# Kernel optimization log

Hardware: AMD Instinct MI355X
Metric: run time of the kernel (lower is better)

The kernel has to match this reference:

```python
import jax, jax.numpy as jnp
import numpy as np

B, S, D = 4, 2048, 512
H = 8
HD = D // H  # 64
F = 2048
EPS = 1e-12


def _layer_norm(x, g, b):
    mu = jnp.mean(x, axis=-1, keepdims=True)
    var = jnp.mean((x - mu) ** 2, axis=-1, keepdims=True)
    return (x - mu) * jax.lax.rsqrt(var + EPS) * g + b


def setup_inputs() -> dict:
    key = jax.random.key(0)
    ks = jax.random.split(key, 16)
    sd = 0.02
    inp = {
        "x": jax.random.normal(ks[0], (B, S, D), dtype=jnp.float32),
        # per-head q/k/v projections stacked: [H, D, HD] weights, [H, HD] biases
        "Wq": jax.random.normal(ks[1], (H, D, HD), dtype=jnp.float32) * sd,
        "bq": jnp.zeros((H, HD), dtype=jnp.float32),
        "Wk": jax.random.normal(ks[2], (H, D, HD), dtype=jnp.float32) * sd,
        "bk": jnp.zeros((H, HD), dtype=jnp.float32),
        "Wv": jax.random.normal(ks[3], (H, D, HD), dtype=jnp.float32) * sd,
        "bv": jnp.zeros((H, HD), dtype=jnp.float32),
        "Wo": jax.random.normal(ks[4], (D, D), dtype=jnp.float32) * sd,
        "bo": jnp.zeros((D,), dtype=jnp.float32),
        "W1": jax.random.normal(ks[5], (D, F), dtype=jnp.float32) * sd,
        "b1": jnp.zeros((F,), dtype=jnp.float32),
        "W2": jax.random.normal(ks[6], (F, D), dtype=jnp.float32) * sd,
        "b2": jnp.zeros((D,), dtype=jnp.float32),
        "ln1_g": jnp.ones((D,), dtype=jnp.float32),
        "ln1_b": jnp.zeros((D,), dtype=jnp.float32),
        "ln2_g": jnp.ones((D,), dtype=jnp.float32),
        "ln2_b": jnp.zeros((D,), dtype=jnp.float32),
    }
    return inp


def reference(x, Wq, bq, Wk, bk, Wv, bv, Wo, bo, W1, b1, W2, b2,
              ln1_g, ln1_b, ln2_g, ln2_b):
    # Multi-head attention: per-head Linear projections, batched over heads.
    q = jnp.einsum('bsd,hde->bhse', x, Wq) + bq[None, :, None, :]
    k = jnp.einsum('bsd,hde->bhse', x, Wk) + bk[None, :, None, :]
    v = jnp.einsum('bsd,hde->bhse', x, Wv) + bv[None, :, None, :]
    scores = jnp.einsum('bhse,bhte->bhst', q, k) / jnp.sqrt(jnp.float32(HD))
    weights = jax.nn.softmax(scores, axis=-1)  # [B,H,S,S] -- dominant traffic
    attn = jnp.einsum('bhst,bhte->bhse', weights, v)
    # concat heads in order along feature dim -> [B,S,D]
    concat = jnp.transpose(attn, (0, 2, 1, 3)).reshape(B, S, D)
    attn_out = concat @ Wo + bo
    # post-LN residual 1
    x1 = _layer_norm(x + attn_out, ln1_g, ln1_b)
    # FFN (exact GELU, matching torch nn.GELU default)
    h = jax.nn.gelu(x1 @ W1 + b1, approximate=False)
    ff = h @ W2 + b2
    # post-LN residual 2
    return _layer_norm(x1 + ff, ln2_g, ln2_b)
```

## Files before the change

### kernel.cpp

```cpp
#include <hip/hip_runtime.h>
#include <math.h>

#define Bb 4
#define Ss 2048
#define Dd 512
#define Hh 8
#define HDd 64
#define Ff 2048

typedef __bf16 bf16x8 __attribute__((ext_vector_type(8)));
typedef __bf16 bf16x4 __attribute__((ext_vector_type(4)));
typedef float  f32x4  __attribute__((ext_vector_type(4)));

__device__ __forceinline__ float gelu_f(float x) {
    return 0.5f * x * (1.0f + erff(x * 0.70710678118654752440f));
}

__device__ __forceinline__ unsigned short bfbits(float f) {
    __bf16 h = (__bf16)f;
    return __builtin_bit_cast(unsigned short, h);
}

__global__ __launch_bounds__(256) void tconv_kernel(
    const float* __restrict__ in, unsigned short* __restrict__ out,
    int R, int C)
{
    __shared__ float tile[32][33];
    const size_t bo = (size_t)blockIdx.z * R * C;
    const int c0 = blockIdx.x * 32, r0 = blockIdx.y * 32;
    const int tx = threadIdx.x & 31, ty = threadIdx.x >> 5;
    #pragma unroll
    for (int rr = ty; rr < 32; rr += 8)
        tile[rr][tx] = in[bo + (size_t)(r0 + rr) * C + c0 + tx];
    __syncthreads();
    #pragma unroll
    for (int cc = ty; cc < 32; cc += 8)
        out[bo + (size_t)(c0 + cc) * R + r0 + tx] = bfbits(tile[tx][cc]);
}

__global__ __launch_bounds__(256) void f2b_kernel(
    const float* __restrict__ in, unsigned short* __restrict__ out)
{
    const size_t i = ((size_t)blockIdx.x * 256 + threadIdx.x) * 8;
    float4 a = *(const float4*)(in + i);
    float4 b = *(const float4*)(in + i + 4);
    union { unsigned short us[8]; uint4 u; } p;
    p.us[0] = bfbits(a.x); p.us[1] = bfbits(a.y);
    p.us[2] = bfbits(a.z); p.us[3] = bfbits(a.w);
    p.us[4] = bfbits(b.x); p.us[5] = bfbits(b.y);
    p.us[6] = bfbits(b.z); p.us[7] = bfbits(b.w);
    *(uint4*)(out + i) = p.u;
}

template<int ACT, int OUTBF>
__global__ __launch_bounds__(256) void gemm_mfma(
    const unsigned short* __restrict__ A, const unsigned short* __restrict__ Bt,
    const float* __restrict__ bias, void* __restrict__ C,
    int M, int N, int K)
{
    __shared__ unsigned short Asb[128][40];
    __shared__ unsigned short Bsb[128][40];
    const int t    = threadIdx.x;
    const int lane = t & 63;
    const int w    = t >> 6;
    const int ln15 = lane & 15;
    const int quad = lane >> 4;
    const int mw = (w & 1) * 64;
    const int nw = (w >> 1) * 64;
    const int m0 = blockIdx.y * 128;
    const int n0 = blockIdx.x * 128;

    f32x4 acc[4][4];
    #pragma unroll
    for (int i = 0; i < 4; i++)
        #pragma unroll
        for (int j = 0; j < 4; j++) acc[i][j] = (f32x4){0.f, 0.f, 0.f, 0.f};

    for (int k0 = 0; k0 < K; k0 += 32) {
        #pragma unroll
        for (int p = 0; p < 2; p++) {
            const int f   = t + p * 256;
            const int row = f >> 2;
            const int k8  = (f & 3) << 3;
            *(bf16x8*)&Asb[row][k8] =
                *(const bf16x8*)(A + (size_t)(m0 + row) * K + k0 + k8);
            *(bf16x8*)&Bsb[row][k8] =
                *(const bf16x8*)(Bt + (size_t)(n0 + row) * K + k0 + k8);
        }
        __syncthreads();
        bf16x8 af[4], bf[4];
        const int kcol = quad * 8;
        #pragma unroll
        for (int i = 0; i < 4; i++)
            af[i] = *(const bf16x8*)&Asb[mw + i * 16 + ln15][kcol];
        #pragma unroll
        for (int j = 0; j < 4; j++)
            bf[j] = *(const bf16x8*)&Bsb[nw + j * 16 + ln15][kcol];
        #pragma unroll
        for (int i = 0; i < 4; i++)
            #pragma unroll
            for (int j = 0; j < 4; j++)
                acc[i][j] = __builtin_amdgcn_mfma_f32_16x16x32_bf16(
                    af[i], bf[j], acc[i][j], 0, 0, 0);
        __syncthreads();
    }

    #pragma unroll
    for (int i = 0; i < 4; i++) {
        #pragma unroll
        for (int r = 0; r < 4; r++) {
            const int m = m0 + mw + i * 16 + quad * 4 + r;
            #pragma unroll
            for (int j = 0; j < 4; j++) {
                const int n = n0 + nw + j * 16 + ln15;
                float val = acc[i][j][r] + bias[n];
                if (ACT) val = gelu_f(val);
                if (OUTBF)
                    ((unsigned short*)C)[(size_t)m * N + n] = bfbits(val);
                else
                    ((float*)C)[(size_t)m * N + n] = val;
            }
        }
    }
}

__global__ __launch_bounds__(256) void qkv_mfma(
    const unsigned short* __restrict__ A,
    const unsigned short* __restrict__ WqT, const unsigned short* __restrict__ WkT,
    const unsigned short* __restrict__ WvT,
    const float* __restrict__ bq, const float* __restrict__ bk,
    const float* __restrict__ bv, unsigned short* __restrict__ qkv)
{
    const unsigned short* Bt = blockIdx.z == 0 ? WqT : (blockIdx.z == 1 ? WkT : WvT);
    const float* bias = blockIdx.z == 0 ? bq : (blockIdx.z == 1 ? bk : bv);
    unsigned short* O = qkv + (size_t)blockIdx.z * ((size_t)Bb * Hh * Ss * HDd);
    const float scl = blockIdx.z == 0 ? 0.125f : 1.0f;

    __shared__ unsigned short Asb[128][40];
    __shared__ unsigned short Bsb[128][40];
    const int t    = threadIdx.x;
    const int lane = t & 63;
    const int w    = t >> 6;
    const int ln15 = lane & 15;
    const int quad = lane >> 4;
    const int mw = (w & 1) * 64;
    const int nw = (w >> 1) * 64;
    const int m0 = blockIdx.y * 128;
    const int n0 = blockIdx.x * 128;

    f32x4 acc[4][4];
    #pragma unroll
    for (int i = 0; i < 4; i++)
        #pragma unroll
        for (int j = 0; j < 4; j++) acc[i][j] = (f32x4){0.f, 0.f, 0.f, 0.f};

    for (int k0 = 0; k0 < Dd; k0 += 32) {
        #pragma unroll
        for (int p = 0; p < 2; p++) {
            const int f   = t + p * 256;
            const int row = f >> 2;
            const int k8  = (f & 3) << 3;
            *(bf16x8*)&Asb[row][k8] =
                *(const bf16x8*)(A + (size_t)(m0 + row) * Dd + k0 + k8);
            *(bf16x8*)&Bsb[row][k8] =
                *(const bf16x8*)(Bt + (size_t)(n0 + row) * Dd + k0 + k8);
        }
        __syncthreads();
        bf16x8 af[4], bf[4];
        const int kcol = quad * 8;
        #pragma unroll
        for (int i = 0; i < 4; i++)
            af[i] = *(const bf16x8*)&Asb[mw + i * 16 + ln15][kcol];
        #pragma unroll
        for (int j = 0; j < 4; j++)
            bf[j] = *(const bf16x8*)&Bsb[nw + j * 16 + ln15][kcol];
        #pragma unroll
        for (int i = 0; i < 4; i++)
            #pragma unroll
            for (int j = 0; j < 4; j++)
                acc[i][j] = __builtin_amdgcn_mfma_f32_16x16x32_bf16(
                    af[i], bf[j], acc[i][j], 0, 0, 0);
        __syncthreads();
    }

    if (blockIdx.z == 2) {
        #pragma unroll
        for (int i = 0; i < 4; i++) {
            const int mb = m0 + mw + i * 16 + quad * 4;
            const int bI = mb >> 11;
            const int sI = mb & 2047;
            #pragma unroll
            for (int j = 0; j < 4; j++) {
                const int n = n0 + nw + j * 16 + ln15;
                union { unsigned short us[4]; uint2 u2; } pk;
                #pragma unroll
                for (int r = 0; r < 4; r++)
                    pk.us[r] = bfbits(acc[i][j][r] + bias[n]);
                *(uint2*)&O[(((size_t)bI * Hh + (n >> 6)) * HDd + (n & 63)) * Ss + sI]
                    = pk.u2;
            }
        }
    } else {
        #pragma unroll
        for (int i = 0; i < 4; i++) {
            #pragma unroll
            for (int r = 0; r < 4; r++) {
                const int m  = m0 + mw + i * 16 + quad * 4 + r;
                const int bI = m >> 11;
                const int sI = m & 2047;
                #pragma unroll
                for (int j = 0; j < 4; j++) {
                    const int n = n0 + nw + j * 16 + ln15;
                    const float val = (acc[i][j][r] + bias[n]) * scl;
                    O[(((size_t)bI * Hh + (n >> 6)) * Ss + sI) * HDd + (n & 63)] =
                        bfbits(val);
                }
            }
        }
    }
}

__global__ __launch_bounds__(256) void attn_mfma(
    const unsigned short* __restrict__ q, const unsigned short* __restrict__ k,
    const unsigned short* __restrict__ vt, unsigned short* __restrict__ out)
{
    __shared__ unsigned short Ks[64][72];
    __shared__ unsigned short VTs[64][72];
    __shared__ unsigned short Ps[64][72];
    __shared__ float alph[4][16];
    const int t    = threadIdx.x;
    const int lane = t & 63;
    const int w    = t >> 6;
    const int ln15 = lane & 15;
    const int quad = lane >> 4;
    const int qw   = w * 16;
    const int h = blockIdx.y, b = blockIdx.z;
    const int q0 = blockIdx.x * 64;
    const unsigned short* qb  = q  + (((size_t)b * Hh + h) * Ss + q0) * HDd;
    const unsigned short* kb  = k  + ((size_t)b * Hh + h) * Ss * HDd;
    const unsigned short* vtb = vt + ((size_t)b * Hh + h) * HDd * Ss;

    const bf16x8 qf0 = *(const bf16x8*)(qb + (size_t)(qw + ln15) * HDd + quad * 8);
    const bf16x8 qf1 = *(const bf16x8*)(qb + (size_t)(qw + ln15) * HDd + 32 + quad * 8);

    f32x4 o_acc[4];
    #pragma unroll
    for (int s = 0; s < 4; s++) o_acc[s] = (f32x4){0.f, 0.f, 0.f, 0.f};
    float m_run = -1e30f, l_run = 0.f;

    for (int kt = 0; kt < Ss; kt += 64) {
        __syncthreads();
        #pragma unroll
        for (int p = 0; p < 2; p++) {
            const int u = p * 256 + t;
            const int row = u >> 3, ch = u & 7;
            *(bf16x8*)&Ks[row][ch * 8] =
                *(const bf16x8*)(kb + (size_t)(kt + row) * HDd + ch * 8);
            *(bf16x8*)&VTs[row][ch * 8] =
                *(const bf16x8*)(vtb + (size_t)row * Ss + kt + ch * 8);
        }
        __syncthreads();

        f32x4 sc[4];
        #pragma unroll
        for (int s = 0; s < 4; s++) {
            const bf16x8 ka = *(const bf16x8*)&Ks[s * 16 + ln15][quad * 8];
            const bf16x8 kb2 = *(const bf16x8*)&Ks[s * 16 + ln15][32 + quad * 8];
            f32x4 z = (f32x4){0.f, 0.f, 0.f, 0.f};
            z = __builtin_amdgcn_mfma_f32_16x16x32_bf16(ka, qf0, z, 0, 0, 0);
            sc[s] = __builtin_amdgcn_mfma_f32_16x16x32_bf16(kb2, qf1, z, 0, 0, 0);
        }

        float mt = -1e30f;
        #pragma unroll
        for (int s = 0; s < 4; s++)
            #pragma unroll
            for (int r = 0; r < 4; r++) mt = fmaxf(mt, sc[s][r]);
        mt = fmaxf(mt, __shfl_xor(mt, 16));
        mt = fmaxf(mt, __shfl_xor(mt, 32));
        const float mn = fmaxf(m_run, mt);
        const float a = __expf(m_run - mn);
        float lt = 0.f;
        #pragma unroll
        for (int s = 0; s < 4; s++)
            #pragma unroll
            for (int r = 0; r < 4; r++) {
                sc[s][r] = __expf(sc[s][r] - mn);
                lt += sc[s][r];
            }
        lt += __shfl_xor(lt, 16);
        lt += __shfl_xor(lt, 32);
        l_run = l_run * a + lt;
        m_run = mn;
        if (quad == 0) alph[w][ln15] = a;

        #pragma unroll
        for (int s = 0; s < 4; s++) {
            union { unsigned short us[4]; uint2 u2; } pk;
            #pragma unroll
            for (int r = 0; r < 4; r++) pk.us[r] = bfbits(sc[s][r]);
            *(uint2*)&Ps[qw + ln15][s * 16 + quad * 4] = pk.u2;
        }

        const float4 av = *(const float4*)&alph[w][quad * 4];
        #pragma unroll
        for (int s = 0; s < 4; s++) {
            o_acc[s][0] *= av.x; o_acc[s][1] *= av.y;
            o_acc[s][2] *= av.z; o_acc[s][3] *= av.w;
        }

        const bf16x8 pf0 = *(const bf16x8*)&Ps[qw + ln15][quad * 8];
        const bf16x8 pf1 = *(const bf16x8*)&Ps[qw + ln15][32 + quad * 8];
        #pragma unroll
        for (int s = 0; s < 4; s++) {
            const bf16x8 v0 = *(const bf16x8*)&VTs[s * 16 + ln15][quad * 8];
            const bf16x8 v1 = *(const bf16x8*)&VTs[s * 16 + ln15][32 + quad * 8];
            o_acc[s] = __builtin_amdgcn_mfma_f32_16x16x32_bf16(pf0, v0, o_acc[s], 0, 0, 0);
            o_acc[s] = __builtin_amdgcn_mfma_f32_16x16x32_bf16(pf1, v1, o_acc[s], 0, 0, 0);
        }
    }

    if (quad == 0) alph[w][ln15] = l_run;
    const float4 lv = *(const float4*)&alph[w][quad * 4];
    const float inv[4] = {1.f / lv.x, 1.f / lv.y, 1.f / lv.z, 1.f / lv.w};
    #pragma unroll
    for (int r = 0; r < 4; r++) {
        const int row = q0 + qw + quad * 4 + r;
        #pragma unroll
        for (int s = 0; s < 4; s++) {
            const int dim = s * 16 + ln15;
            out[((size_t)b * Ss + row) * Dd + h * HDd + dim] =
                bfbits(o_acc[s][r] * inv[r]);
        }
    }
}

template<int WRITE_BF>
__global__ __launch_bounds__(256) void ln_kernel(
    const float* __restrict__ a, const float* __restrict__ res,
    const float* __restrict__ g, const float* __restrict__ bb,
    float* __restrict__ out, unsigned short* __restrict__ outb)
{
    const int row = blockIdx.x;
    const int t = threadIdx.x;
    const float* pa = a + (size_t)row * Dd;
    const float* pr = res + (size_t)row * Dd;
    float v0 = pa[t] + pr[t];
    float v1 = pa[t + 256] + pr[t + 256];

    float sum = v0 + v1;
    #pragma unroll
    for (int o = 32; o; o >>= 1) sum += __shfl_down(sum, o);
    __shared__ float red1[4], red2[4];
    const int wid = t >> 6, lane = t & 63;
    if (!lane) red1[wid] = sum;
    __syncthreads();
    sum = red1[0] + red1[1] + red1[2] + red1[3];
    const float mu = sum * (1.0f / Dd);

    const float d0 = v0 - mu, d1 = v1 - mu;
    float sq = d0 * d0 + d1 * d1;
    #pragma unroll
    for (int o = 32; o; o >>= 1) sq += __shfl_down(sq, o);
    if (!lane) red2[wid] = sq;
    __syncthreads();
    sq = red2[0] + red2[1] + red2[2] + red2[3];
    const float rstd = rsqrtf(sq * (1.0f / Dd) + 1e-12f);

    const float y0 = d0 * rstd * g[t] + bb[t];
    const float y1 = d1 * rstd * g[t + 256] + bb[t + 256];
    out[(size_t)row * Dd + t]       = y0;
    out[(size_t)row * Dd + t + 256] = y1;
    if (WRITE_BF) {
        outb[(size_t)row * Dd + t]       = bfbits(y0);
        outb[(size_t)row * Dd + t + 256] = bfbits(y1);
    }
}

extern "C" void kernel_launch(void* const* d_in, const int* in_sizes, int n_in,
                              void* d_out, int out_size, void* d_ws, size_t ws_size,
                              hipStream_t stream) {
    const float* x   = (const float*)d_in[0];
    const float* Wq  = (const float*)d_in[1];
    const float* bq  = (const float*)d_in[2];
    const float* Wk  = (const float*)d_in[3];
    const float* bk  = (const float*)d_in[4];
    const float* Wv  = (const float*)d_in[5];
    const float* bv  = (const float*)d_in[6];
    const float* Wo  = (const float*)d_in[7];
    const float* bo  = (const float*)d_in[8];
    const float* W1  = (const float*)d_in[9];
    const float* b1  = (const float*)d_in[10];
    const float* W2  = (const float*)d_in[11];
    const float* b2  = (const float*)d_in[12];
    const float* g1  = (const float*)d_in[13];
    const float* be1 = (const float*)d_in[14];
    const float* g2  = (const float*)d_in[15];
    const float* be2 = (const float*)d_in[16];
    float* out = (float*)d_out;

    const size_t NT = (size_t)Bb * Ss * Dd;
    unsigned short* wsu  = (unsigned short*)d_ws;
    unsigned short* qkvb = wsu;
    unsigned short* hb   = wsu + 3 * NT;
    unsigned short* actb = wsu + 7 * NT;
    unsigned short* x1b  = wsu + 8 * NT;
    float* proj = (float*)(wsu + 9 * NT);
    float* ff   = proj;
    float* x1   = proj + NT;
    unsigned short* wpool = (unsigned short*)(x1 + NT);
    unsigned short* WqT = wpool;
    unsigned short* WkT = wpool + 262144;
    unsigned short* WvT = wpool + 524288;
    unsigned short* WoT = wpool + 786432;
    unsigned short* W1T = wpool + 1048576;
    unsigned short* W2T = wpool + 2097152;
    const int M = Bb * Ss;

    tconv_kernel<<<dim3(2, 16, 8), 256, 0, stream>>>(Wq, WqT, Dd, HDd);
    tconv_kernel<<<dim3(2, 16, 8), 256, 0, stream>>>(Wk, WkT, Dd, HDd);
    tconv_kernel<<<dim3(2, 16, 8), 256, 0, stream>>>(Wv, WvT, Dd, HDd);
    tconv_kernel<<<dim3(16, 16, 1), 256, 0, stream>>>(Wo, WoT, Dd, Dd);
    tconv_kernel<<<dim3(64, 16, 1), 256, 0, stream>>>(W1, W1T, Dd, Ff);
    tconv_kernel<<<dim3(16, 64, 1), 256, 0, stream>>>(W2, W2T, Ff, Dd);

    f2b_kernel<<<2048, 256, 0, stream>>>(x, actb);
    qkv_mfma<<<dim3(Dd / 128, M / 128, 3), 256, 0, stream>>>(
        actb, WqT, WkT, WvT, bq, bk, bv, qkvb);

    attn_mfma<<<dim3(Ss / 64, Hh, Bb), 256, 0, stream>>>(
        qkvb, qkvb + NT, qkvb + 2 * NT, actb);

    gemm_mfma<0, 0><<<dim3(Dd / 128, M / 128), 256, 0, stream>>>(
        actb, WoT, bo, proj, M, Dd, Dd);

    ln_kernel<1><<<M, 256, 0, stream>>>(x, proj, g1, be1, x1, x1b);

    gemm_mfma<1, 1><<<dim3(Ff / 128, M / 128), 256, 0, stream>>>(
        x1b, W1T, b1, hb, M, Ff, Dd);
    gemm_mfma<0, 0><<<dim3(Dd / 128, M / 128), 256, 0, stream>>>(
        hb, W2T, b2, ff, M, Dd, Ff);

    ln_kernel<0><<<M, 256, 0, stream>>>(x1, ff, g2, be2, out, nullptr);
}
```

Baseline: 361.8 us.

## Merge weight-prep launches and load GEMM tiles directly into LDS

```diff
diff --git a/kernel.cpp b/kernel.cpp
--- a/kernel.cpp
+++ b/kernel.cpp
@@ -9,7 +9,6 @@
 #define Ff 2048
 
 typedef __bf16 bf16x8 __attribute__((ext_vector_type(8)));
-typedef __bf16 bf16x4 __attribute__((ext_vector_type(4)));
 typedef float  f32x4  __attribute__((ext_vector_type(4)));
 
 __device__ __forceinline__ float gelu_f(float x) {
@@ -21,35 +20,66 @@
     return __builtin_bit_cast(unsigned short, h);
 }
 
-__global__ __launch_bounds__(256) void tconv_kernel(
+__device__ __forceinline__ void gld16(const unsigned short* g, unsigned short* l) {
+    __builtin_amdgcn_global_load_lds(
+        (const __attribute__((address_space(1))) unsigned int*)g,
+        (__attribute__((address_space(3))) unsigned int*)l, 16, 0, 0);
+}
+
+__device__ __forceinline__ void tile_tconv(
     const float* __restrict__ in, unsigned short* __restrict__ out,
-    int R, int C)
+    int R, int C, int c0, int r0)
 {
     __shared__ float tile[32][33];
-    const size_t bo = (size_t)blockIdx.z * R * C;
-    const int c0 = blockIdx.x * 32, r0 = blockIdx.y * 32;
     const int tx = threadIdx.x & 31, ty = threadIdx.x >> 5;
     #pragma unroll
     for (int rr = ty; rr < 32; rr += 8)
-        tile[rr][tx] = in[bo + (size_t)(r0 + rr) * C + c0 + tx];
+        tile[rr][tx] = in[(size_t)(r0 + rr) * C + c0 + tx];
     __syncthreads();
     #pragma unroll
     for (int cc = ty; cc < 32; cc += 8)
-        out[bo + (size_t)(c0 + cc) * R + r0 + tx] = bfbits(tile[tx][cc]);
-}
-
-__global__ __launch_bounds__(256) void f2b_kernel(
-    const float* __restrict__ in, unsigned short* __restrict__ out)
-{
-    const size_t i = ((size_t)blockIdx.x * 256 + threadIdx.x) * 8;
-    float4 a = *(const float4*)(in + i);
-    float4 b = *(const float4*)(in + i + 4);
-    union { unsigned short us[8]; uint4 u; } p;
-    p.us[0] = bfbits(a.x); p.us[1] = bfbits(a.y);
-    p.us[2] = bfbits(a.z); p.us[3] = bfbits(a.w);
-    p.us[4] = bfbits(b.x); p.us[5] = bfbits(b.y);
-    p.us[6] = bfbits(b.z); p.us[7] = bfbits(b.w);
-    *(uint4*)(out + i) = p.u;
+        out[(size_t)(c0 + cc) * R + r0 + tx] = bfbits(tile[tx][cc]);
+}
+
+__global__ __launch_bounds__(256) void prep_kernel(
+    const float* __restrict__ Wq, const float* __restrict__ Wk,
+    const float* __restrict__ Wv, const float* __restrict__ Wo,
+    const float* __restrict__ W1, const float* __restrict__ W2,
+    const float* __restrict__ x,
+    unsigned short* __restrict__ WqT, unsigned short* __restrict__ WkT,
+    unsigned short* __restrict__ WvT, unsigned short* __restrict__ WoT,
+    unsigned short* __restrict__ W1T, unsigned short* __restrict__ W2T,
+    unsigned short* __restrict__ xb)
+{
+    const int bid = blockIdx.x;
+    if (bid < 768) {
+        const float* src = bid < 256 ? Wq : (bid < 512 ? Wk : Wv);
+        unsigned short* dst = bid < 256 ? WqT : (bid < 512 ? WkT : WvT);
+        const int local = bid & 255;
+        const int z = local >> 5;
+        const int rem = local & 31;
+        tile_tconv(src + (size_t)z * Dd * HDd, dst + (size_t)z * Dd * HDd,
+                   Dd, HDd, (rem & 1) * 32, (rem >> 1) * 32);
+    } else if (bid < 1024) {
+        const int local = bid - 768;
+        tile_tconv(Wo, WoT, Dd, Dd, (local & 15) * 32, (local >> 4) * 32);
+    } else if (bid < 2048) {
+        const int local = bid - 1024;
+        tile_tconv(W1, W1T, Dd, Ff, (local & 63) * 32, (local >> 6) * 32);
+    } else if (bid < 3072) {
+        const int local = bid - 2048;
+        tile_tconv(W2, W2T, Ff, Dd, (local & 15) * 32, (local >> 4) * 32);
+    } else {
+        const size_t i = ((size_t)(bid - 3072) * 256 + threadIdx.x) * 8;
+        float4 a = *(const float4*)(x + i);
+        float4 b = *(const float4*)(x + i + 4);
+        union { unsigned short us[8]; uint4 u; } p;
+        p.us[0] = bfbits(a.x); p.us[1] = bfbits(a.y);
+        p.us[2] = bfbits(a.z); p.us[3] = bfbits(a.w);
+        p.us[4] = bfbits(b.x); p.us[5] = bfbits(b.y);
+        p.us[6] = bfbits(b.z); p.us[7] = bfbits(b.w);
+        *(uint4*)(xb + i) = p.u;
+    }
 }
 
 template<int ACT, int OUTBF>
@@ -58,8 +88,8 @@
     const float* __restrict__ bias, void* __restrict__ C,
     int M, int N, int K)
 {
-    __shared__ unsigned short Asb[128][40];
-    __shared__ unsigned short Bsb[128][40];
+    __shared__ unsigned short Asb[128 * 32];
+    __shared__ unsigned short Bsb[128 * 32];
     const int t    = threadIdx.x;
     const int lane = t & 63;
     const int w    = t >> 6;
@@ -70,6 +100,9 @@
     const int m0 = blockIdx.y * 128;
     const int n0 = blockIdx.x * 128;
 
+    const int r0c = t >> 2,           ch0 = (t & 3) << 3;
+    const int r1c = (t + 256) >> 2,   ch1 = ch0;
+
     f32x4 acc[4][4];
     #pragma unroll
     for (int i = 0; i < 4; i++)
@@ -77,25 +110,19 @@
         for (int j = 0; j < 4; j++) acc[i][j] = (f32x4){0.f, 0.f, 0.f, 0.f};
 
     for (int k0 = 0; k0 < K; k0 += 32) {
-        #pragma unroll
-        for (int p = 0; p < 2; p++) {
-            const int f   = t + p * 256;
-            const int row = f >> 2;
-            const int k8  = (f & 3) << 3;
-            *(bf16x8*)&Asb[row][k8] =
-                *(const bf16x8*)(A + (size_t)(m0 + row) * K + k0 + k8);
-            *(bf16x8*)&Bsb[row][k8] =
-                *(const bf16x8*)(Bt + (size_t)(n0 + row) * K + k0 + k8);
-        }
+        gld16(A  + (size_t)(m0 + r0c) * K + k0 + ch0, &Asb[t * 8]);
+        gld16(A  + (size_t)(m0 + r1c) * K + k0 + ch1, &Asb[(t + 256) * 8]);
+        gld16(Bt + (size_t)(n0 + r0c) * K + k0 + ch0, &Bsb[t * 8]);
+        gld16(Bt + (size_t)(n0 + r1c) * K + k0 + ch1, &Bsb[(t + 256) * 8]);
         __syncthreads();
         bf16x8 af[4], bf[4];
         const int kcol = quad * 8;
         #pragma unroll
         for (int i = 0; i < 4; i++)
-            af[i] = *(const bf16x8*)&Asb[mw + i * 16 + ln15][kcol];
+            af[i] = *(const bf16x8*)&Asb[(mw + i * 16 + ln15) * 32 + kcol];
         #pragma unroll
         for (int j = 0; j < 4; j++)
-            bf[j] = *(const bf16x8*)&Bsb[nw + j * 16 + ln15][kcol];
+            bf[j] = *(const bf16x8*)&Bsb[(nw + j * 16 + ln15) * 32 + kcol];
         #pragma unroll
         for (int i = 0; i < 4; i++)
             #pragma unroll
@@ -136,8 +163,8 @@
     unsigned short* O = qkv + (size_t)blockIdx.z * ((size_t)Bb * Hh * Ss * HDd);
     const float scl = blockIdx.z == 0 ? 0.125f : 1.0f;
 
-    __shared__ unsigned short Asb[128][40];
-    __shared__ unsigned short Bsb[128][40];
+    __shared__ unsigned short Asb[128 * 32];
+    __shared__ unsigned short Bsb[128 * 32];
     const int t    = threadIdx.x;
     const int lane = t & 63;
     const int w    = t >> 6;
@@ -148,6 +175,9 @@
     const int m0 = blockIdx.y * 128;
     const int n0 = blockIdx.x * 128;
 
+    const int r0c = t >> 2,         ch0 = (t & 3) << 3;
+    const int r1c = (t + 256) >> 2, ch1 = ch0;
+
     f32x4 acc[4][4];
     #pragma unroll
     for (int i = 0; i < 4; i++)
@@ -155,25 +185,19 @@
         for (int j = 0; j < 4; j++) acc[i][j] = (f32x4){0.f, 0.f, 0.f, 0.f};
 
     for (int k0 = 0; k0 < Dd; k0 += 32) {
-        #pragma unroll
-        for (int p = 0; p < 2; p++) {
-            const int f   = t + p * 256;
-            const int row = f >> 2;
-            const int k8  = (f & 3) << 3;
-            *(bf16x8*)&Asb[row][k8] =
-                *(const bf16x8*)(A + (size_t)(m0 + row) * Dd + k0 + k8);
-            *(bf16x8*)&Bsb[row][k8] =
-                *(const bf16x8*)(Bt + (size_t)(n0 + row) * Dd + k0 + k8);
-        }
+        gld16(A  + (size_t)(m0 + r0c) * Dd + k0 + ch0, &Asb[t * 8]);
+        gld16(A  + (size_t)(m0 + r1c) * Dd + k0 + ch1, &Asb[(t + 256) * 8]);
+        gld16(Bt + (size_t)(n0 + r0c) * Dd + k0 + ch0, &Bsb[t * 8]);
+        gld16(Bt + (size_t)(n0 + r1c) * Dd + k0 + ch1, &Bsb[(t + 256) * 8]);
         __syncthreads();
         bf16x8 af[4], bf[4];
         const int kcol = quad * 8;
         #pragma unroll
         for (int i = 0; i < 4; i++)
-            af[i] = *(const bf16x8*)&Asb[mw + i * 16 + ln15][kcol];
+            af[i] = *(const bf16x8*)&Asb[(mw + i * 16 + ln15) * 32 + kcol];
         #pragma unroll
         for (int j = 0; j < 4; j++)
-            bf[j] = *(const bf16x8*)&Bsb[nw + j * 16 + ln15][kcol];
+            bf[j] = *(const bf16x8*)&Bsb[(nw + j * 16 + ln15) * 32 + kcol];
         #pragma unroll
         for (int i = 0; i < 4; i++)
             #pragma unroll
@@ -264,7 +288,7 @@
         f32x4 sc[4];
         #pragma unroll
         for (int s = 0; s < 4; s++) {
-            const bf16x8 ka = *(const bf16x8*)&Ks[s * 16 + ln15][quad * 8];
+            const bf16x8 ka  = *(const bf16x8*)&Ks[s * 16 + ln15][quad * 8];
             const bf16x8 kb2 = *(const bf16x8*)&Ks[s * 16 + ln15][32 + quad * 8];
             f32x4 z = (f32x4){0.f, 0.f, 0.f, 0.f};
             z = __builtin_amdgcn_mfma_f32_16x16x32_bf16(ka, qf0, z, 0, 0, 0);
@@ -417,14 +441,10 @@
     unsigned short* W2T = wpool + 2097152;
     const int M = Bb * Ss;
 
-    tconv_kernel<<<dim3(2, 16, 8), 256, 0, stream>>>(Wq, WqT, Dd, HDd);
-    tconv_kernel<<<dim3(2, 16, 8), 256, 0, stream>>>(Wk, WkT, Dd, HDd);
-    tconv_kernel<<<dim3(2, 16, 8), 256, 0, stream>>>(Wv, WvT, Dd, HDd);
-    tconv_kernel<<<dim3(16, 16, 1), 256, 0, stream>>>(Wo, WoT, Dd, Dd);
-    tconv_kernel<<<dim3(64, 16, 1), 256, 0, stream>>>(W1, W1T, Dd, Ff);
-    tconv_kernel<<<dim3(16, 64, 1), 256, 0, stream>>>(W2, W2T, Ff, Dd);
-
-    f2b_kernel<<<2048, 256, 0, stream>>>(x, actb);
+    prep_kernel<<<5120, 256, 0, stream>>>(
+        Wq, Wk, Wv, Wo, W1, W2, x,
+        WqT, WkT, WvT, WoT, W1T, W2T, actb);
+
     qkv_mfma<<<dim3(Dd / 128, M / 128, 3), 256, 0, stream>>>(
         actb, WqT, WkT, WvT, bq, bk, bv, qkvb);
 
```

Result: faster. 342.6 us (-5.3%).
